# Performance work log

Measured on AMD Instinct MI355X. Metric: run time of the kernel, lower is better.

The kernel has to match this reference:

```python
import jax, jax.numpy as jnp
import numpy as np

VOCAB_SIZE = 32000

def _factorize(vocab_size):
    f = int(np.round(np.sqrt(vocab_size)))
    while vocab_size % f != 0:
        f += 1
    return f, vocab_size // f  # (vocab_factor, vocab_chunk) = (200, 160)

VOCAB_FACTOR, VOCAB_CHUNK = _factorize(VOCAB_SIZE)

def setup_inputs() -> dict:
    key = jax.random.key(0)
    logits = jax.random.normal(key, (4, 2048, VOCAB_SIZE), dtype=jnp.float32)
    return {"logits": logits}

def reference(logits):
    B, S, V = logits.shape
    N = B * S
    # full softmax over vocab, viewed as [N, vocab_factor, vocab_chunk]
    probs = jax.nn.softmax(jax.lax.stop_gradient(logits).astype(jnp.float32), axis=-1)
    factored = probs.reshape(N, VOCAB_FACTOR, VOCAB_CHUNK)
    # stage 1: sample outer chunk from chunk-sum marginals
    outer_probs = factored.sum(axis=-1)                       # [N, VOCAB_FACTOR]
    k1, k2 = jax.random.split(jax.random.key(42))
    outer_sample = jax.random.categorical(k1, jnp.log(outer_probs), axis=-1)  # [N]
    # stage 2: gather the sampled chunk, sample within it
    inner_probs = jnp.take_along_axis(
        factored, outer_sample[:, None, None], axis=1)[:, 0, :]  # [N, VOCAB_CHUNK]
    inner_sample = jax.random.categorical(k2, jnp.log(inner_probs), axis=-1)  # [N]
    sample = VOCAB_CHUNK * outer_sample + inner_sample
    return sample.reshape(B, S)
```

## Files before the change

### kernel.cpp

```cpp
#include <hip/hip_runtime.h>
#include <stdint.h>

#define PARTITIONABLE 1

constexpr int V  = 32000;
constexpr int F  = 200;
constexpr int C  = 160;
constexpr int NT = 512;

__device__ __forceinline__ uint32_t rotl32(uint32_t x, uint32_t r) {
  return (x << r) | (x >> (32u - r));
}

__device__ __forceinline__ void threefry2x32(uint32_t ka, uint32_t kb,
                                             uint32_t x0, uint32_t x1,
                                             uint32_t& o0, uint32_t& o1) {
  const uint32_t ks2 = ka ^ kb ^ 0x1BD11BDAu;
  x0 += ka; x1 += kb;
#define TF_R4(a,b,c,d) \
  x0 += x1; x1 = rotl32(x1, a); x1 ^= x0; \
  x0 += x1; x1 = rotl32(x1, b); x1 ^= x0; \
  x0 += x1; x1 = rotl32(x1, c); x1 ^= x0; \
  x0 += x1; x1 = rotl32(x1, d); x1 ^= x0;
  TF_R4(13,15,26,6)  x0 += kb;  x1 += ks2 + 1u;
  TF_R4(17,29,16,24) x0 += ks2; x1 += ka  + 2u;
  TF_R4(13,15,26,6)  x0 += ka;  x1 += kb  + 3u;
  TF_R4(17,29,16,24) x0 += kb;  x1 += ks2 + 4u;
  TF_R4(13,15,26,6)  x0 += ks2; x1 += ka  + 5u;
#undef TF_R4
  o0 = x0; o1 = x1;
}

__device__ __forceinline__ uint32_t rand_bits(uint32_t ka, uint32_t kb,
                                              uint32_t idx, uint32_t half) {
  uint32_t o0, o1;
#if PARTITIONABLE
  (void)half;
  threefry2x32(ka, kb, 0u, idx, o0, o1);
  return o0 ^ o1;
#else
  if (idx < half) { threefry2x32(ka, kb, idx, idx + half, o0, o1); return o0; }
  else            { threefry2x32(ka, kb, idx - half, idx, o0, o1); return o1; }
#endif
}

__device__ __forceinline__ float bits_to_gumbel(uint32_t bits) {
  float u = __uint_as_float((bits >> 9) | 0x3f800000u) - 1.0f;
  u = fmaxf(u, 1.1754943508222875e-38f);
  return -logf(-logf(u));
}

__device__ __forceinline__ unsigned long long pack_max(float z, int idx) {
  uint32_t ub = __float_as_uint(z);
  ub = (ub & 0x80000000u) ? ~ub : (ub | 0x80000000u);
  return ((unsigned long long)ub << 32) | (uint32_t)(0xFFFFFFFFu - (uint32_t)idx);
}

__global__ __launch_bounds__(NT)
void sampler_kernel(const float* __restrict__ logits, int* __restrict__ out) {
  const int row = blockIdx.x;
  const float* rp = logits + (size_t)row * V;
  const int t    = threadIdx.x;
  const int lane = t & 63;
  const int wid  = t >> 6;

  constexpr float LOG2E = 1.4426950408889634f;
  constexpr float SHIFT = 64.0f;
  constexpr float LN2   = 0.6931471805599453f;

  __shared__ float css[F];
  __shared__ float wred[NT / 64];
  __shared__ unsigned long long amax1, amax2;

  if (t == 0) { amax1 = 0ull; amax2 = 0ull; }

  uint32_t k1a, k1b, k2a, k2b;
#if PARTITIONABLE
  threefry2x32(0u, 42u, 0u, 0u, k1a, k1b);
  threefry2x32(0u, 42u, 0u, 1u, k2a, k2b);
#else
  {
    uint32_t a0, b0, a1, b1;
    threefry2x32(0u, 42u, 0u, 2u, a0, b0);
    threefry2x32(0u, 42u, 1u, 3u, a1, b1);
    k1a = a0; k1b = a1; k2a = b0; k2b = b1;
  }
#endif

  const int g  = t >> 3;
  const int gl = t & 7;
  for (int c = g; c < F; c += NT / 8) {
    const float4* cp4 = (const float4*)(rp + c * C);
    float4 w[5];
#pragma unroll
    for (int j = 0; j < 5; ++j) w[j] = cp4[gl + 8 * j];
    float s = 0.f;
#pragma unroll
    for (int j = 0; j < 5; ++j) {
      s += __builtin_amdgcn_exp2f(fmaf(w[j].x, LOG2E, -SHIFT));
      s += __builtin_amdgcn_exp2f(fmaf(w[j].y, LOG2E, -SHIFT));
      s += __builtin_amdgcn_exp2f(fmaf(w[j].z, LOG2E, -SHIFT));
      s += __builtin_amdgcn_exp2f(fmaf(w[j].w, LOG2E, -SHIFT));
    }
#pragma unroll
    for (int o = 4; o; o >>= 1) s += __shfl_xor(s, o);
    if (gl == 0) css[c] = s;
  }
  __syncthreads();

  float myCs = (t < F) ? css[t] : 0.f;
  {
    float v = myCs;
#pragma unroll
    for (int o = 32; o; o >>= 1) v += __shfl_xor(v, o);
    if (lane == 0) wred[wid] = v;
  }
  __syncthreads();
  float S = wred[0];
#pragma unroll
  for (int w = 1; w < NT / 64; ++w) S += wred[w];

  if (t < F) {
    float l1 = logf(myCs / S);
    uint32_t idx = (uint32_t)(row * F + t);
    float gu = bits_to_gumbel(rand_bits(k1a, k1b, idx, (uint32_t)(gridDim.x * F / 2)));
    atomicMax(&amax1, pack_max(l1 + gu, t));
  }
  __syncthreads();
  const int outer = (int)(0xFFFFFFFFu - (uint32_t)(amax1 & 0xFFFFFFFFull));

  if (t < C) {
    float v   = rp[outer * C + t];
    float lnZ = logf(S) + SHIFT * LN2;
    float l2  = v - lnZ;
    uint32_t idx = (uint32_t)(row * C + t);
    float gu = bits_to_gumbel(rand_bits(k2a, k2b, idx, (uint32_t)(gridDim.x * C / 2)));
    atomicMax(&amax2, pack_max(l2 + gu, t));
  }
  __syncthreads();
  if (t == 0) {
    int inner = (int)(0xFFFFFFFFu - (uint32_t)(amax2 & 0xFFFFFFFFull));
    out[row] = C * outer + inner;
  }
}

extern "C" void kernel_launch(void* const* d_in, const int* in_sizes, int n_in,
                              void* d_out, int out_size, void* d_ws, size_t ws_size,
                              hipStream_t stream) {
  const float* logits = (const float*)d_in[0];
  int* out = (int*)d_out;
  const int N = in_sizes[0] / V;
  sampler_kernel<<<N, NT, 0, stream>>>(logits, out);
}
```

Before: 179.2 us.

## Split sampler into persistent chunk-sum streaming kernel and warp-per-row sample kernel

Replaces the one-block-per-row fused kernel with two kernels when workspace allows. A persistent grid of 1024 blocks streams all row-chunk pairs and writes chunk sums to workspace. A second kernel then handles one row per wavefront, doing the two Gumbel-max stages with shuffle reductions instead of shared-memory atomics. The aim is better load balance and less per-block sync overhead on the memory-bound pass, at the cost of an extra launch and a workspace round trip. The old fused path is kept as a fallback and the unused non-partitionable RNG branch is removed.

```diff
diff --git a/kernel.cpp b/kernel.cpp
--- a/kernel.cpp
+++ b/kernel.cpp
@@ -7,6 +7,10 @@
 constexpr int F  = 200;
 constexpr int C  = 160;
 constexpr int NT = 512;
+
+constexpr float LOG2E = 1.4426950408889634f;
+constexpr float SHIFT = 64.0f;
+constexpr float LN2   = 0.6931471805599453f;
 
 __device__ __forceinline__ uint32_t rotl32(uint32_t x, uint32_t r) {
   return (x << r) | (x >> (32u - r));
@@ -31,17 +35,10 @@
   o0 = x0; o1 = x1;
 }
 
-__device__ __forceinline__ uint32_t rand_bits(uint32_t ka, uint32_t kb,
-                                              uint32_t idx, uint32_t half) {
+__device__ __forceinline__ uint32_t rand_bits(uint32_t ka, uint32_t kb, uint32_t idx) {
   uint32_t o0, o1;
-#if PARTITIONABLE
-  (void)half;
   threefry2x32(ka, kb, 0u, idx, o0, o1);
   return o0 ^ o1;
-#else
-  if (idx < half) { threefry2x32(ka, kb, idx, idx + half, o0, o1); return o0; }
-  else            { threefry2x32(ka, kb, idx - half, idx, o0, o1); return o1; }
-#endif
 }
 
 __device__ __forceinline__ float bits_to_gumbel(uint32_t bits) {
@@ -56,36 +53,115 @@
   return ((unsigned long long)ub << 32) | (uint32_t)(0xFFFFFFFFu - (uint32_t)idx);
 }
 
+__device__ __forceinline__ void derive_keys(uint32_t& k1a, uint32_t& k1b,
+                                            uint32_t& k2a, uint32_t& k2b) {
+  threefry2x32(0u, 42u, 0u, 0u, k1a, k1b);
+  threefry2x32(0u, 42u, 0u, 1u, k2a, k2b);
+}
+
 __global__ __launch_bounds__(NT)
-void sampler_kernel(const float* __restrict__ logits, int* __restrict__ out) {
+void stream_kernel(const float* __restrict__ logits, float* __restrict__ css,
+                   int n_tasks) {
+  const int gl      = threadIdx.x & 7;
+  const int grp     = (blockIdx.x * NT + threadIdx.x) >> 3;
+  const int n_grps  = (gridDim.x * NT) >> 3;
+  for (int task = grp; task < n_tasks; task += n_grps) {
+    const int row = task / F;
+    const int c   = task - row * F;
+    const float4* cp4 = (const float4*)(logits + (size_t)row * V + c * C);
+    float4 w[5];
+#pragma unroll
+    for (int j = 0; j < 5; ++j) w[j] = cp4[gl + 8 * j];
+    float s = 0.f;
+#pragma unroll
+    for (int j = 0; j < 5; ++j) {
+      s += __builtin_amdgcn_exp2f(fmaf(w[j].x, LOG2E, -SHIFT));
+      s += __builtin_amdgcn_exp2f(fmaf(w[j].y, LOG2E, -SHIFT));
+      s += __builtin_amdgcn_exp2f(fmaf(w[j].z, LOG2E, -SHIFT));
+      s += __builtin_amdgcn_exp2f(fmaf(w[j].w, LOG2E, -SHIFT));
+    }
+#pragma unroll
+    for (int o = 4; o; o >>= 1) s += __shfl_xor(s, o);
+    if (gl == 0) css[task] = s;
+  }
+}
+
+__global__ __launch_bounds__(NT)
+void sample_kernel(const float* __restrict__ logits, const float* __restrict__ css,
+                   int* __restrict__ out, int n_rows) {
+  const int lane = threadIdx.x & 63;
+  const int row  = blockIdx.x * (NT / 64) + (threadIdx.x >> 6);
+  if (row >= n_rows) return;
+
+  uint32_t k1a, k1b, k2a, k2b;
+  derive_keys(k1a, k1b, k2a, k2b);
+
+  float4 c4 = make_float4(0.f, 0.f, 0.f, 0.f);
+  if (lane < 50) c4 = ((const float4*)(css + (size_t)row * F))[lane];
+
+  float S = (c4.x + c4.y) + (c4.z + c4.w);
+#pragma unroll
+  for (int o = 32; o; o >>= 1) S += __shfl_xor(S, o);
+
+  unsigned long long best = 0ull;
+  if (lane < 50) {
+    const float cs[4] = {c4.x, c4.y, c4.z, c4.w};
+#pragma unroll
+    for (int k = 0; k < 4; ++k) {
+      int f = lane * 4 + k;
+      float z = logf(cs[k] / S) +
+                bits_to_gumbel(rand_bits(k1a, k1b, (uint32_t)(row * F + f)));
+      unsigned long long p = pack_max(z, f);
+      best = (p > best) ? p : best;
+    }
+  }
+#pragma unroll
+  for (int o = 32; o; o >>= 1) {
+    unsigned long long q = __shfl_xor(best, o);
+    best = (q > best) ? q : best;
+  }
+  const int outer = (int)(0xFFFFFFFFu - (uint32_t)(best & 0xFFFFFFFFull));
+
+  const float lnZ = logf(S) + SHIFT * LN2;
+  unsigned long long best2 = 0ull;
+  if (lane < 40) {
+    float4 v4 = ((const float4*)(logits + (size_t)row * V + outer * C))[lane];
+    const float v[4] = {v4.x, v4.y, v4.z, v4.w};
+#pragma unroll
+    for (int k = 0; k < 4; ++k) {
+      int c = lane * 4 + k;
+      float z = (v[k] - lnZ) +
+                bits_to_gumbel(rand_bits(k2a, k2b, (uint32_t)(row * C + c)));
+      unsigned long long p = pack_max(z, c);
+      best2 = (p > best2) ? p : best2;
+    }
+  }
+#pragma unroll
+  for (int o = 32; o; o >>= 1) {
+    unsigned long long q = __shfl_xor(best2, o);
+    best2 = (q > best2) ? q : best2;
+  }
+  if (lane == 0) {
+    int inner = (int)(0xFFFFFFFFu - (uint32_t)(best2 & 0xFFFFFFFFull));
+    out[row] = C * outer + inner;
+  }
+}
+
+__global__ __launch_bounds__(NT)
+void fused_kernel(const float* __restrict__ logits, int* __restrict__ out) {
   const int row = blockIdx.x;
   const float* rp = logits + (size_t)row * V;
   const int t    = threadIdx.x;
   const int lane = t & 63;
   const int wid  = t >> 6;
 
-  constexpr float LOG2E = 1.4426950408889634f;
-  constexpr float SHIFT = 64.0f;
-  constexpr float LN2   = 0.6931471805599453f;
-
   __shared__ float css[F];
   __shared__ float wred[NT / 64];
   __shared__ unsigned long long amax1, amax2;
-
   if (t == 0) { amax1 = 0ull; amax2 = 0ull; }
 
   uint32_t k1a, k1b, k2a, k2b;
-#if PARTITIONABLE
-  threefry2x32(0u, 42u, 0u, 0u, k1a, k1b);
-  threefry2x32(0u, 42u, 0u, 1u, k2a, k2b);
-#else
-  {
-    uint32_t a0, b0, a1, b1;
-    threefry2x32(0u, 42u, 0u, 2u, a0, b0);
-    threefry2x32(0u, 42u, 1u, 3u, a1, b1);
-    k1a = a0; k1b = a1; k2a = b0; k2b = b1;
-  }
-#endif
+  derive_keys(k1a, k1b, k2a, k2b);
 
   const int g  = t >> 3;
   const int gl = t & 7;
@@ -122,8 +198,7 @@
 
   if (t < F) {
     float l1 = logf(myCs / S);
-    uint32_t idx = (uint32_t)(row * F + t);
-    float gu = bits_to_gumbel(rand_bits(k1a, k1b, idx, (uint32_t)(gridDim.x * F / 2)));
+    float gu = bits_to_gumbel(rand_bits(k1a, k1b, (uint32_t)(row * F + t)));
     atomicMax(&amax1, pack_max(l1 + gu, t));
   }
   __syncthreads();
@@ -132,10 +207,8 @@
   if (t < C) {
     float v   = rp[outer * C + t];
     float lnZ = logf(S) + SHIFT * LN2;
-    float l2  = v - lnZ;
-    uint32_t idx = (uint32_t)(row * C + t);
-    float gu = bits_to_gumbel(rand_bits(k2a, k2b, idx, (uint32_t)(gridDim.x * C / 2)));
-    atomicMax(&amax2, pack_max(l2 + gu, t));
+    float gu  = bits_to_gumbel(rand_bits(k2a, k2b, (uint32_t)(row * C + t)));
+    atomicMax(&amax2, pack_max((v - lnZ) + gu, t));
   }
   __syncthreads();
   if (t == 0) {
@@ -150,5 +223,12 @@
   const float* logits = (const float*)d_in[0];
   int* out = (int*)d_out;
   const int N = in_sizes[0] / V;
-  sampler_kernel<<<N, NT, 0, stream>>>(logits, out);
-}
+  const size_t need = (size_t)N * F * sizeof(float);
+  if (ws_size >= need) {
+    float* css = (float*)d_ws;
+    stream_kernel<<<1024, NT, 0, stream>>>(logits, css, N * F);
+    sample_kernel<<<(N + NT / 64 - 1) / (NT / 64), NT, 0, stream>>>(logits, css, out, N);
+  } else {
+    fused_kernel<<<N, NT, 0, stream>>>(logits, out);
+  }
+}
```

Measured after the change: 210.1 us. +17.2%, slower.
